# Kernel optimization log

Hardware: AMD Instinct MI355X
Metric: run time of the kernel (lower is better)

Reference implementation:

```python
import jax, jax.numpy as jnp
import numpy as np

IN_FEATURES = 8192
OUT_FEATURES = 28672
BATCH = 8  # tokens; skinny GEMM -> memory-bound weight streaming


def setup_inputs() -> dict:
    key = jax.random.key(0)
    k1, k2, k3, k4 = jax.random.split(key, 4)
    x = jax.random.normal(k1, (BATCH, IN_FEATURES), dtype=jnp.float32)
    # ternary codes in {0,1,2} -> weight values {-1,0,+1}; pack 4 codes / byte
    codes = jax.random.randint(k2, (OUT_FEATURES, IN_FEATURES), 0, 3, dtype=jnp.int32)
    codes4 = codes.reshape(OUT_FEATURES, IN_FEATURES // 4, 4)
    shifts = jnp.array([0, 2, 4, 6], dtype=jnp.int32)
    packed_weight = jnp.sum(codes4 << shifts, axis=-1).astype(jnp.int32)  # [O, I//4]
    weight_scale = jax.random.uniform(k3, (1,), dtype=jnp.float32, minval=0.01, maxval=0.1)
    bias = jax.random.normal(k4, (OUT_FEATURES,), dtype=jnp.float32)
    return {"x": x, "packed_weight": packed_weight, "weight_scale": weight_scale, "bias": bias}


def _unpack_ternary(packed):
    # [O, I//4] int -> [O, I] ternary in {-1,0,1}
    shifts = jnp.array([0, 2, 4, 6], dtype=jnp.int32)
    w = ((packed[:, :, None] >> shifts) & 3) - 1  # [O, I//4, 4]
    return w.reshape(packed.shape[0], -1)


def reference(x, packed_weight, weight_scale, bias):
    B = x.shape[0]
    x_flat = x.reshape(B, IN_FEATURES)
    # per-tensor absmax int8 activation quantization
    absmax = jnp.maximum(jnp.max(jnp.abs(x_flat)), 1e-5)
    act_scale = absmax / 127.0
    x_q = jnp.clip(jnp.round(x_flat / act_scale), -128, 127)  # int8 values, kept f32
    w = _unpack_ternary(packed_weight).astype(jnp.float32)  # [O, I]
    # fused dequant GEMM: integer-valued accumulation, single scalar scale
    acc = jnp.einsum('bi,oi->bo', x_q, w)  # exact in f32 (|acc| << 2^24)
    scale = weight_scale[0] * act_scale
    out = acc * scale + bias
    return out.reshape(B, OUT_FEATURES)
```

## Files before the change

kernel.cpp:

```cpp
#include <hip/hip_runtime.h>
#include <stdint.h>

#define O_FEATS 28672
#define I_FEATS 8192
#define BATCH 8
#define WPR 2048


#if __has_builtin(__builtin_amdgcn_sdot4)
#define DOT4(a, b, c) __builtin_amdgcn_sdot4((a), (b), (c), false)
#else
static __device__ __forceinline__ int dot4_sw(int a, int b, int c) {
  c += (int)(signed char)(a & 0xff) * (int)(signed char)(b & 0xff);
  c += (int)(signed char)((a >> 8) & 0xff) * (int)(signed char)((b >> 8) & 0xff);
  c += (int)(signed char)((a >> 16) & 0xff) * (int)(signed char)((b >> 16) & 0xff);
  c += (int)(signed char)((a >> 24) & 0xff) * (int)(signed char)((b >> 24) & 0xff);
  return c;
}
#define DOT4(a, b, c) dot4_sw((a), (b), (c))
#endif

static __device__ __forceinline__ int unpack4(uint32_t p) {
  uint32_t lo = p & 0x0Fu;
  uint32_t hi = (p >> 4) & 0x0Fu;
  uint32_t a = (lo * 0x41u) & 0x0303u;
  uint32_t b = (hi * 0x41u) & 0x0303u;
  return (int)(a | (b << 16));
}

__global__ void k_init(uint32_t* __restrict__ ws) {
  int t = threadIdx.x;
  if (t == 0) ws[0] = 0u;
  if (t >= 4 && t < 12) ws[t] = 0u;
}

__global__ void k_absmax(const float* __restrict__ x, uint32_t* __restrict__ ws) {
  int idx = blockIdx.x * 256 + threadIdx.x;
  float4 v = ((const float4*)x)[idx];
  float m = fmaxf(fmaxf(fabsf(v.x), fabsf(v.y)), fmaxf(fabsf(v.z), fabsf(v.w)));
#pragma unroll
  for (int off = 32; off; off >>= 1)
    m = fmaxf(m, __shfl_xor(m, off));
  if ((threadIdx.x & 63) == 0)
    atomicMax(ws, __float_as_uint(m));
}

__global__ void k_quant(const float* __restrict__ x, uint32_t* __restrict__ ws) {
  int b = blockIdx.x >> 3, seg = blockIdx.x & 7;
  int t = threadIdx.x;
  float amax = fmaxf(__uint_as_float(ws[0]), 1e-5f);
  float s = amax / 127.0f;
  float4 v = ((const float4*)(x + b * I_FEATS + seg * 1024))[t];
  int q0 = (int)fminf(fmaxf(rintf(v.x / s), -128.f), 127.f);
  int q1 = (int)fminf(fmaxf(rintf(v.y / s), -128.f), 127.f);
  int q2 = (int)fminf(fmaxf(rintf(v.z / s), -128.f), 127.f);
  int q3 = (int)fminf(fmaxf(rintf(v.w / s), -128.f), 127.f);
  uint32_t pk = (uint32_t)(q0 & 0xff) | ((uint32_t)(q1 & 0xff) << 8) |
                ((uint32_t)(q2 & 0xff) << 16) | ((uint32_t)(q3 & 0xff) << 24);
  ws[64 + b * 2048 + seg * 256 + t] = pk;
  int s4 = q0 + q1 + q2 + q3;
#pragma unroll
  for (int off = 32; off; off >>= 1)
    s4 += __shfl_xor(s4, off);
  if ((t & 63) == 0)
    atomicAdd((int*)ws + 4 + b, s4);
}

__global__ void __launch_bounds__(256, 2)
k_gemm(const int* __restrict__ Wp, const float* __restrict__ wscale,
       const float* __restrict__ bias, const uint32_t* __restrict__ ws,
       float* __restrict__ out) {
  __shared__ uint32_t xq_lds[BATCH * 2048];

  int t = threadIdx.x;
  {
    const int4* src = (const int4*)(ws + 64);
    int4* dst = (int4*)xq_lds;
#pragma unroll
    for (int i = 0; i < 16; ++i) dst[t + 256 * i] = src[t + 256 * i];
  }
  __syncthreads();

  const int wave = t >> 6, lane = t & 63;
  const int o_base = blockIdx.x * 16 + wave * 4;

  int4 wcur[4], wnxt[4];
#pragma unroll
  for (int oo = 0; oo < 4; ++oo)
    wcur[oo] = *(const int4*)(Wp + (o_base + oo) * WPR + 4 * lane);

  int acc[4][8];
#pragma unroll
  for (int oo = 0; oo < 4; ++oo)
#pragma unroll
    for (int b = 0; b < 8; ++b) acc[oo][b] = 0;

#pragma unroll
  for (int j = 0; j < 8; ++j) {
    const int cc = j * 64 + lane;
    if (j < 7) {
#pragma unroll
      for (int oo = 0; oo < 4; ++oo)
        wnxt[oo] = *(const int4*)(Wp + (o_base + oo) * WPR + 4 * (cc + 64));
    }
    int code[4][4];
#pragma unroll
    for (int oo = 0; oo < 4; ++oo) {
      const uint32_t* pw = (const uint32_t*)&wcur[oo];
#pragma unroll
      for (int m = 0; m < 4; ++m)
        code[oo][m] = unpack4(pw[m]);
    }
#pragma unroll
    for (int b = 0; b < 8; ++b) {
      int4 xv = *(const int4*)&xq_lds[b * 2048 + 4 * cc];
#pragma unroll
      for (int oo = 0; oo < 4; ++oo) {
        acc[oo][b] = DOT4(code[oo][0], xv.x, acc[oo][b]);
        acc[oo][b] = DOT4(code[oo][1], xv.y, acc[oo][b]);
        acc[oo][b] = DOT4(code[oo][2], xv.z, acc[oo][b]);
        acc[oo][b] = DOT4(code[oo][3], xv.w, acc[oo][b]);
      }
    }
#pragma unroll
    for (int oo = 0; oo < 4; ++oo) wcur[oo] = wnxt[oo];
  }

  int v[32];
#pragma unroll
  for (int oo = 0; oo < 4; ++oo)
#pragma unroll
    for (int b = 0; b < 8; ++b) v[oo * 8 + b] = acc[oo][b];
#pragma unroll
  for (int s = 0; s < 5; ++s) {
    const int m = 1 << s;
    const int n = 16 >> s;
    const bool up = (lane & m) != 0;
#pragma unroll
    for (int i = 0; i < n; ++i) {
      int give = up ? v[i] : v[i + n];
      int keep = up ? v[i + n] : v[i];
      v[i] = keep + __shfl_xor(give, m);
    }
  }
  int tot = v[0] + __shfl_xor(v[0], 32);

  if (lane < 32) {
    int h = ((lane & 1) << 4) | ((lane & 2) << 2) | (lane & 4) |
            ((lane & 8) >> 2) | ((lane & 16) >> 4);
    int oo = h >> 3, b = h & 7;
    float amax = fmaxf(__uint_as_float(ws[0]), 1e-5f);
    float scale = (amax / 127.0f) * wscale[0];
    int sumx = ((const int*)ws)[4 + b];
    int o = o_base + oo;
    out[b * O_FEATS + o] = (float)(tot - sumx) * scale + bias[o];
  }
}

extern "C" void kernel_launch(void* const* d_in, const int* in_sizes, int n_in,
                              void* d_out, int out_size, void* d_ws, size_t ws_size,
                              hipStream_t stream) {
  const float* x = (const float*)d_in[0];
  const int* pw = (const int*)d_in[1];
  const float* wscale = (const float*)d_in[2];
  const float* bias = (const float*)d_in[3];
  float* out = (float*)d_out;
  uint32_t* ws = (uint32_t*)d_ws;

  k_init<<<1, 64, 0, stream>>>(ws);
  k_absmax<<<64, 256, 0, stream>>>(x, ws);
  k_quant<<<64, 256, 0, stream>>>(x, ws);
  k_gemm<<<1792, 256, 0, stream>>>(pw, wscale, bias, ws, out);
}
```

Baseline: 369.5 us.

## Use persistent tile loop in GEMM and replace atomics with per-block partials

```diff
diff --git a/kernel.cpp b/kernel.cpp
--- a/kernel.cpp
+++ b/kernel.cpp
@@ -5,6 +5,8 @@
 #define I_FEATS 8192
 #define BATCH 8
 #define WPR 2048
+#define NTILES 1792
+#define GRID 512
 
 
 #if __has_builtin(__builtin_amdgcn_sdot4)
@@ -20,36 +22,47 @@
 #define DOT4(a, b, c) dot4_sw((a), (b), (c))
 #endif
 
-static __device__ __forceinline__ int unpack4(uint32_t p) {
+static __device__ __forceinline__ uint32_t unpack4(uint32_t p) {
   uint32_t lo = p & 0x0Fu;
   uint32_t hi = (p >> 4) & 0x0Fu;
   uint32_t a = (lo * 0x41u) & 0x0303u;
   uint32_t b = (hi * 0x41u) & 0x0303u;
-  return (int)(a | (b << 16));
-}
-
-__global__ void k_init(uint32_t* __restrict__ ws) {
+  return a | (b << 16);
+}
+
+__global__ void k_absmax(const float* __restrict__ x, uint32_t* __restrict__ ws) {
+  __shared__ float red[4];
   int t = threadIdx.x;
-  if (t == 0) ws[0] = 0u;
-  if (t >= 4 && t < 12) ws[t] = 0u;
-}
-
-__global__ void k_absmax(const float* __restrict__ x, uint32_t* __restrict__ ws) {
-  int idx = blockIdx.x * 256 + threadIdx.x;
-  float4 v = ((const float4*)x)[idx];
+  float4 v = ((const float4*)x)[blockIdx.x * 256 + t];
   float m = fmaxf(fmaxf(fabsf(v.x), fabsf(v.y)), fmaxf(fabsf(v.z), fabsf(v.w)));
 #pragma unroll
   for (int off = 32; off; off >>= 1)
     m = fmaxf(m, __shfl_xor(m, off));
-  if ((threadIdx.x & 63) == 0)
-    atomicMax(ws, __float_as_uint(m));
+  if ((t & 63) == 0) red[t >> 6] = m;
+  __syncthreads();
+  if (t == 0)
+    ws[16 + blockIdx.x] =
+        __float_as_uint(fmaxf(fmaxf(red[0], red[1]), fmaxf(red[2], red[3])));
 }
 
 __global__ void k_quant(const float* __restrict__ x, uint32_t* __restrict__ ws) {
+  __shared__ float s_amax;
+  __shared__ int reds[4];
   int b = blockIdx.x >> 3, seg = blockIdx.x & 7;
   int t = threadIdx.x;
-  float amax = fmaxf(__uint_as_float(ws[0]), 1e-5f);
-  float s = amax / 127.0f;
+  if (t < 64) {
+    float m = __uint_as_float(ws[16 + t]);
+#pragma unroll
+    for (int off = 32; off; off >>= 1)
+      m = fmaxf(m, __shfl_xor(m, off));
+    if (t == 0) {
+      float a = fmaxf(m, 1e-5f);
+      s_amax = a;
+      ws[0] = __float_as_uint(a);
+    }
+  }
+  __syncthreads();
+  float s = s_amax / 127.0f;
   float4 v = ((const float4*)(x + b * I_FEATS + seg * 1024))[t];
   int q0 = (int)fminf(fmaxf(rintf(v.x / s), -128.f), 127.f);
   int q1 = (int)fminf(fmaxf(rintf(v.y / s), -128.f), 127.f);
@@ -57,13 +70,15 @@
   int q3 = (int)fminf(fmaxf(rintf(v.w / s), -128.f), 127.f);
   uint32_t pk = (uint32_t)(q0 & 0xff) | ((uint32_t)(q1 & 0xff) << 8) |
                 ((uint32_t)(q2 & 0xff) << 16) | ((uint32_t)(q3 & 0xff) << 24);
-  ws[64 + b * 2048 + seg * 256 + t] = pk;
+  ws[1024 + b * 2048 + seg * 256 + t] = pk;
   int s4 = q0 + q1 + q2 + q3;
 #pragma unroll
   for (int off = 32; off; off >>= 1)
     s4 += __shfl_xor(s4, off);
-  if ((t & 63) == 0)
-    atomicAdd((int*)ws + 4 + b, s4);
+  if ((t & 63) == 0) reds[t >> 6] = s4;
+  __syncthreads();
+  if (t == 0)
+    ws[128 + blockIdx.x] = (uint32_t)(reds[0] + reds[1] + reds[2] + reds[3]);
 }
 
 __global__ void __launch_bounds__(256, 2)
@@ -71,89 +86,112 @@
        const float* __restrict__ bias, const uint32_t* __restrict__ ws,
        float* __restrict__ out) {
   __shared__ uint32_t xq_lds[BATCH * 2048];
+  __shared__ uint32_t lut[256];
+  __shared__ int s_sumx[BATCH];
+  __shared__ float s_scale;
 
   int t = threadIdx.x;
   {
-    const int4* src = (const int4*)(ws + 64);
+    const int4* src = (const int4*)(ws + 1024);
     int4* dst = (int4*)xq_lds;
 #pragma unroll
     for (int i = 0; i < 16; ++i) dst[t + 256 * i] = src[t + 256 * i];
   }
+  lut[t] = unpack4((uint32_t)t);
+  if (t < 64) {
+    int p = (int)ws[128 + t];
+    p += __shfl_xor(p, 1);
+    p += __shfl_xor(p, 2);
+    p += __shfl_xor(p, 4);
+    if ((t & 7) == 0) s_sumx[t >> 3] = p;
+  }
+  if (t == 0) s_scale = (__uint_as_float(ws[0]) / 127.0f) * wscale[0];
   __syncthreads();
 
   const int wave = t >> 6, lane = t & 63;
-  const int o_base = blockIdx.x * 16 + wave * 4;
+
+  int tiles[4];
+  int ntile = 0;
+  for (int tt = blockIdx.x; tt < NTILES; tt += GRID) tiles[ntile++] = tt;
 
   int4 wcur[4], wnxt[4];
-#pragma unroll
-  for (int oo = 0; oo < 4; ++oo)
-    wcur[oo] = *(const int4*)(Wp + (o_base + oo) * WPR + 4 * lane);
-
-  int acc[4][8];
-#pragma unroll
-  for (int oo = 0; oo < 4; ++oo)
-#pragma unroll
-    for (int b = 0; b < 8; ++b) acc[oo][b] = 0;
-
-#pragma unroll
-  for (int j = 0; j < 8; ++j) {
-    const int cc = j * 64 + lane;
-    if (j < 7) {
-#pragma unroll
-      for (int oo = 0; oo < 4; ++oo)
-        wnxt[oo] = *(const int4*)(Wp + (o_base + oo) * WPR + 4 * (cc + 64));
-    }
-    int code[4][4];
-#pragma unroll
-    for (int oo = 0; oo < 4; ++oo) {
-      const uint32_t* pw = (const uint32_t*)&wcur[oo];
-#pragma unroll
-      for (int m = 0; m < 4; ++m)
-        code[oo][m] = unpack4(pw[m]);
-    }
-#pragma unroll
-    for (int b = 0; b < 8; ++b) {
-      int4 xv = *(const int4*)&xq_lds[b * 2048 + 4 * cc];
+  {
+    const int* wp0 = Wp + (tiles[0] * 16 + wave * 4) * WPR + 4 * lane;
+#pragma unroll
+    for (int oo = 0; oo < 4; ++oo) wcur[oo] = *(const int4*)(wp0 + oo * WPR);
+  }
+
+  for (int nt = 0; nt < ntile; ++nt) {
+    const int o_base = tiles[nt] * 16 + wave * 4;
+    const int* wp = Wp + o_base * WPR;
+
+    int acc[4][8];
+#pragma unroll
+    for (int oo = 0; oo < 4; ++oo)
+#pragma unroll
+      for (int b = 0; b < 8; ++b) acc[oo][b] = 0;
+
+#pragma unroll
+    for (int j = 0; j < 8; ++j) {
+      const int cc = j * 64 + lane;
+      if (j < 7) {
+#pragma unroll
+        for (int oo = 0; oo < 4; ++oo)
+          wnxt[oo] = *(const int4*)(wp + oo * WPR + 4 * (cc + 64));
+      } else if (nt + 1 < ntile) {
+        const int* wpn = Wp + (tiles[nt + 1] * 16 + wave * 4) * WPR + 4 * lane;
+#pragma unroll
+        for (int oo = 0; oo < 4; ++oo) wnxt[oo] = *(const int4*)(wpn + oo * WPR);
+      }
+      int code[4][4];
 #pragma unroll
       for (int oo = 0; oo < 4; ++oo) {
-        acc[oo][b] = DOT4(code[oo][0], xv.x, acc[oo][b]);
-        acc[oo][b] = DOT4(code[oo][1], xv.y, acc[oo][b]);
-        acc[oo][b] = DOT4(code[oo][2], xv.z, acc[oo][b]);
-        acc[oo][b] = DOT4(code[oo][3], xv.w, acc[oo][b]);
-      }
-    }
-#pragma unroll
-    for (int oo = 0; oo < 4; ++oo) wcur[oo] = wnxt[oo];
-  }
-
-  int v[32];
-#pragma unroll
-  for (int oo = 0; oo < 4; ++oo)
-#pragma unroll
-    for (int b = 0; b < 8; ++b) v[oo * 8 + b] = acc[oo][b];
-#pragma unroll
-  for (int s = 0; s < 5; ++s) {
-    const int m = 1 << s;
-    const int n = 16 >> s;
-    const bool up = (lane & m) != 0;
-#pragma unroll
-    for (int i = 0; i < n; ++i) {
-      int give = up ? v[i] : v[i + n];
-      int keep = up ? v[i + n] : v[i];
-      v[i] = keep + __shfl_xor(give, m);
-    }
-  }
-  int tot = v[0] + __shfl_xor(v[0], 32);
-
-  if (lane < 32) {
-    int h = ((lane & 1) << 4) | ((lane & 2) << 2) | (lane & 4) |
-            ((lane & 8) >> 2) | ((lane & 16) >> 4);
-    int oo = h >> 3, b = h & 7;
-    float amax = fmaxf(__uint_as_float(ws[0]), 1e-5f);
-    float scale = (amax / 127.0f) * wscale[0];
-    int sumx = ((const int*)ws)[4 + b];
-    int o = o_base + oo;
-    out[b * O_FEATS + o] = (float)(tot - sumx) * scale + bias[o];
+        const uint32_t* pw = (const uint32_t*)&wcur[oo];
+#pragma unroll
+        for (int m = 0; m < 4; ++m) code[oo][m] = (int)lut[pw[m] & 0xFFu];
+      }
+#pragma unroll
+      for (int b = 0; b < 8; ++b) {
+        int4 xv = *(const int4*)&xq_lds[b * 2048 + 4 * cc];
+#pragma unroll
+        for (int oo = 0; oo < 4; ++oo) {
+          acc[oo][b] = DOT4(code[oo][0], xv.x, acc[oo][b]);
+          acc[oo][b] = DOT4(code[oo][1], xv.y, acc[oo][b]);
+          acc[oo][b] = DOT4(code[oo][2], xv.z, acc[oo][b]);
+          acc[oo][b] = DOT4(code[oo][3], xv.w, acc[oo][b]);
+        }
+      }
+#pragma unroll
+      for (int oo = 0; oo < 4; ++oo) wcur[oo] = wnxt[oo];
+    }
+
+    int v[32];
+#pragma unroll
+    for (int oo = 0; oo < 4; ++oo)
+#pragma unroll
+      for (int b = 0; b < 8; ++b) v[oo * 8 + b] = acc[oo][b];
+#pragma unroll
+    for (int s = 0; s < 5; ++s) {
+      const int m = 1 << s;
+      const int n = 16 >> s;
+      const bool up = (lane & m) != 0;
+#pragma unroll
+      for (int i = 0; i < n; ++i) {
+        int give = up ? v[i] : v[i + n];
+        int keep = up ? v[i + n] : v[i];
+        v[i] = keep + __shfl_xor(give, m);
+      }
+    }
+    int tot = v[0] + __shfl_xor(v[0], 32);
+
+    if (lane < 32) {
+      int h = ((lane & 1) << 4) | ((lane & 2) << 2) | (lane & 4) |
+              ((lane & 8) >> 2) | ((lane & 16) >> 4);
+      int oo = h >> 3, b = h & 7;
+      int o = o_base + oo;
+      out[b * O_FEATS + o] =
+          (float)(tot - s_sumx[b]) * s_scale + bias[o];
+    }
   }
 }
 
@@ -167,8 +205,7 @@
   float* out = (float*)d_out;
   uint32_t* ws = (uint32_t*)d_ws;
 
-  k_init<<<1, 64, 0, stream>>>(ws);
   k_absmax<<<64, 256, 0, stream>>>(x, ws);
   k_quant<<<64, 256, 0, stream>>>(x, ws);
-  k_gemm<<<1792, 256, 0, stream>>>(pw, wscale, bias, ws, out);
-}
+  k_gemm<<<GRID, 256, 0, stream>>>(pw, wscale, bias, ws, out);
+}
```

Result: slower. 465.8 us (+26.1%).
